# Kernel optimization log

Hardware: AMD Instinct MI355X
Metric: run time of the kernel (lower is better)

## Reference

```python
import jax, jax.numpy as jnp
import numpy as np

# Constants mirroring __init__ kwargs
SOURCE_LABEL = 2.0
SINK_LABEL = 3.0
GM_LABEL = 1.0  # hard-coded as `image == 1` in the torch module
THRESH = 0.05
MAX_ITERS = 500


def setup_inputs() -> dict:
    key = jax.random.key(0)
    # Label volume: 0=background, 1=gray matter, 2=source, 3=sink
    image = jax.random.randint(key, (2, 1, 64, 64, 64), 0, 4).astype(jnp.float32)
    return {"image": image}


def _solve(image):
    bs = image.shape[0]
    # squeeze channel, zero-pad each volume by 1 voxel, concat along axis 0
    vol = jnp.pad(image[:, 0], ((0, 0), (1, 1), (1, 1), (1, 1)))  # (bs, D+2, H+2, W+2)
    vol = vol.reshape(-1, vol.shape[2], vol.shape[3])              # (bs*(D+2), H+2, W+2)
    h, w, d = vol.shape
    wopt = 2.0 / (1.0 + np.pi / float(min(h, w, d)))

    # boundary conditions: 0 at source (already 0), 1 at sink
    init = jnp.where(vol == SINK_LABEL, 1.0, 0.0).astype(jnp.float32)

    # red-black coloring restricted to gray-matter voxels
    ii, jj, kk = jnp.meshgrid(jnp.arange(h), jnp.arange(w), jnp.arange(d), indexing="ij")
    parity = (ii + jj + kk) % 2
    gm = (vol == GM_LABEL)
    black = ((parity == 0) & gm).ravel()
    red = ((parity == 1) & gm).ravel()

    flat0 = init.ravel()

    def nbsum(x):
        # flat-index neighbor gathers x[i-1], x[i+1], x[i-d], x[i+d], x[i-d*w], x[i+d*w]
        # roll(x, s)[i] == x[i - s]; colored voxels never sit at flat boundaries
        return (jnp.roll(x, 1) + jnp.roll(x, -1)
                + jnp.roll(x, d) + jnp.roll(x, -d)
                + jnp.roll(x, d * w) + jnp.roll(x, -d * w))

    def half_step(x, mask):
        adj = wopt * (nbsum(x) - 6.0 * x) / 6.0
        x_new = jnp.where(mask, x + adj, x)
        dv = jnp.sum(jnp.abs(jnp.where(mask, adj, 0.0)))
        return x_new, dv

    def body(carry):
        x, it, _ = carry
        x, dv_b = half_step(x, black)   # black sweep uses pre-sweep values
        x, dv_r = half_step(x, red)     # red sweep uses updated black values
        return x, it + 1, dv_b + dv_r

    def cond(carry):
        _, it, dv = carry
        # torch loop breaks when delta_v < thresh or iterations > 500 (checked post-body)
        return (it == 0) | ((dv >= THRESH) & (it <= MAX_ITERS))

    x, iters, dv = jax.lax.while_loop(
        cond, body, (flat0, jnp.int32(0), jnp.float32(0.0)))

    # split concatenated solution back per-volume and crop the padding
    lap = x.reshape(bs, h // bs, w, d)[:, 1:-1, 1:-1, 1:-1][:, None]  # (bs,1,D,H,W)
    return lap, iters, dv


def reference(image):
    return _solve(image)
```

## Files before the change

### kernel.cpp

```cpp
#include <hip/hip_runtime.h>
#include <cstdint>


#define NBLK 132
#define NTHR 1024
#define NW   (NTHR / 64)

constexpr int NJK   = 66;
constexpr int PLANE = 66 * 66;
constexpr int HPL   = PLANE / 2;
constexpr int NI    = 132;
constexpr int CAPL  = 2048;
constexpr int NOUT  = 2 * 64 * 64 * 64;
constexpr int CTRL_U64 = 408 * 16;
constexpr unsigned long long CNT1   = 1ull << 44;
constexpr unsigned long long MASK44 = CNT1 - 1ull;

__global__ void sor_init_ctrl(unsigned long long* ctrl) {
  for (int i = threadIdx.x; i < CTRL_U64; i += blockDim.x) ctrl[i] = 0ull;
}

__device__ __forceinline__ float cloadf(const float* p) {
  return __hip_atomic_load(p, __ATOMIC_RELAXED, __HIP_MEMORY_SCOPE_AGENT);
}
__device__ __forceinline__ void cstoref(float* p, float v) {
  __hip_atomic_store(p, v, __ATOMIC_RELAXED, __HIP_MEMORY_SCOPE_AGENT);
}
__device__ __forceinline__ unsigned long long cloadu(const unsigned long long* p) {
  return __hip_atomic_load(p, __ATOMIC_RELAXED, __HIP_MEMORY_SCOPE_AGENT);
}
__device__ __forceinline__ void cstoreu(unsigned long long* p, unsigned long long v) {
  __hip_atomic_store(p, v, __ATOMIC_RELAXED, __HIP_MEMORY_SCOPE_AGENT);
}

__device__ __forceinline__ int pad_label_idx(int ii, int jj, int kk) {
  int b  = (ii >= 66) ? 1 : 0;
  int pz = ii - 66 * b;
  if (pz < 1 || pz > 64 || jj < 1 || jj > 64 || kk < 1 || kk > 64) return -1;
  return ((b * 64 + (pz - 1)) * 64 + (jj - 1)) * 64 + (kk - 1);
}

__global__ __launch_bounds__(NTHR, 1)
void sor_main(const float* __restrict__ img,
              float* __restrict__ pb0, float* __restrict__ pb1,
              float* __restrict__ pr0, float* __restrict__ pr1,
              unsigned long long* __restrict__ ctrl,
              float* __restrict__ out) {
  __shared__ double P1[PLANE];
  __shared__ unsigned lsB[CAPL], lsR[CAPL];
  __shared__ unsigned wsum[NW], woff[NW];
  __shared__ unsigned tot;
  __shared__ double redw[NW];
  __shared__ unsigned long long prevs[8];
  __shared__ double sh_dv;

  const int tid = threadIdx.x, bid = blockIdx.x;
  const int lane = tid & 63, wid = tid >> 6;
  const int z = bid;
  const int zm = (z > 0) ? (z - 1) : z;
  const int zp = (z < NI - 1) ? (z + 1) : z;

  for (int o = tid; o < PLANE; o += NTHR) {
    int j = o / NJK, k = o - j * NJK;
    int li = pad_label_idx(z, j, k);
    float L = (li >= 0) ? img[li] : 0.0f;
    P1[o] = (L == 3.0f) ? 1.0 : 0.0;
  }
  if (tid < 8) prevs[tid] = 0ull;

  int cntB = 0, cntR = 0;
  const int CH = (PLANE + NTHR - 1) / NTHR;
  for (int pass = 0; pass < 2; ++pass) {
    unsigned* list = (pass == 0) ? lsB : lsR;
    int c0 = tid * CH;
    int c1 = (c0 + CH < PLANE) ? (c0 + CH) : PLANE;
    unsigned cnt = 0;
    for (int o = c0; o < c1; ++o) {
      int j = o / NJK, k = o - j * NJK;
      if (((z + j + k) & 1) != pass) continue;
      int li = pad_label_idx(z, j, k);
      float L = (li >= 0) ? img[li] : 0.0f;
      if (L == 1.0f) cnt++;
    }
    unsigned incl = cnt;
    #pragma unroll
    for (int m = 1; m < 64; m <<= 1) {
      unsigned t = __shfl_up(incl, m, 64);
      if (lane >= m) incl += t;
    }
    __syncthreads();
    if (lane == 63) wsum[wid] = incl;
    __syncthreads();
    if (tid == 0) {
      unsigned a = 0;
      for (int w = 0; w < NW; ++w) { unsigned c = wsum[w]; woff[w] = a; a += c; }
      tot = a;
    }
    __syncthreads();
    unsigned p = (incl - cnt) + woff[wid];
    for (int o = c0; o < c1; ++o) {
      int j = o / NJK, k = o - j * NJK;
      if (((z + j + k) & 1) != pass) continue;
      int li = pad_label_idx(z, j, k);
      float L = (li >= 0) ? img[li] : 0.0f;
      if (L == 1.0f)
        list[p++] = (unsigned)o | ((unsigned)(33 * j + (k >> 1)) << 16);
    }
    __syncthreads();
    if (pass == 0) cntB = (int)tot; else cntR = (int)tot;
  }

  for (int c = tid; c < HPL; c += NTHR) {
    int j = c / 33, m = c - 33 * j;
    int kb = (m << 1) + ((z + j) & 1);
    int kr = (m << 1) + ((z + j + 1) & 1);
    float vb = (float)P1[NJK * j + kb];
    float vr = (float)P1[NJK * j + kr];
    cstoref(&pb0[(size_t)z * HPL + c], vb);
    cstoref(&pb1[(size_t)z * HPL + c], vb);
    cstoref(&pr0[(size_t)z * HPL + c], vr);
    cstoref(&pr1[(size_t)z * HPL + c], vr);
  }
  __syncthreads();
  if (tid == 0)
    __hip_atomic_fetch_add(&ctrl[(128u + (unsigned)(bid & 15)) * 16u], 1ull,
                           __ATOMIC_RELAXED, __HIP_MEMORY_SCOPE_AGENT);
  if (tid < 16) {
    for (;;) {
      unsigned long long v = cloadu(&ctrl[(128u + (unsigned)tid) * 16u]);
      v += __shfl_xor(v, 1, 64);  v += __shfl_xor(v, 2, 64);
      v += __shfl_xor(v, 4, 64);  v += __shfl_xor(v, 8, 64);
      if (v >= (unsigned long long)NBLK) break;
      __builtin_amdgcn_s_sleep(1);
    }
  }
  __syncthreads();

  const double WOPT = 2.0 / (1.0 + 3.14159265358979323846 / 66.0);

  int itout = 0;
  double dvout = 0.0;

  for (int t = 1; t <= 555; ++t) {
    const float* __restrict__ prold = (t & 1) ? pr0 : pr1;
    float* __restrict__ pbcur       = (t & 1) ? pb1 : pb0;
    float* __restrict__ prcur       = (t & 1) ? pr1 : pr0;

    if (t > 1) {
      const int g = t - 2;
      if (wid == 0 && lane < 2) {
        int nz = (lane == 0) ? (z - 1) : (z + 1);
        if (nz >= 0 && nz < NI) {
          while (cloadu(&ctrl[(276u + (unsigned)nz) * 16u])
                 < (unsigned long long)(t - 1))
            __builtin_amdgcn_s_sleep(1);
        }
      }
      if (g >= 1 && wid == 1 && lane < 16) {
        const int r = g & 7;
        const unsigned n = ((unsigned)g + 7u) >> 3;
        const unsigned long long t64 =
            ((unsigned long long)(132u * n)) << 44;
        unsigned long long v;
        for (;;) {
          v = cloadu(&ctrl[((unsigned)r * 16u + (unsigned)lane) * 16u]);
          v += __shfl_xor(v, 1, 64);  v += __shfl_xor(v, 2, 64);
          v += __shfl_xor(v, 4, 64);  v += __shfl_xor(v, 8, 64);
          if (v >= t64) break;
          __builtin_amdgcn_s_sleep(1);
        }
        if (lane == 0) {
          unsigned long long cum = v & MASK44;
          sh_dv = (double)(cum - prevs[r]) * (1.0 / 1048576.0);
          prevs[r] = cum;
        }
      }
      __syncthreads();
      if (g >= 1) {
        double dvg = sh_dv;
        if (!((dvg >= 0.05) && (g <= 500))) { itout = g; dvout = dvg; break; }
      }
    }

    double acc = 0.0;
    {
      const float* __restrict__ rm = prold + (size_t)zm * HPL;
      const float* __restrict__ rp = prold + (size_t)zp * HPL;
      float* __restrict__ pbz = pbcur + (size_t)z * HPL;
      for (int p = tid; p < cntB; p += NTHR) {
        const unsigned e = lsB[p];
        const int o = (int)(e & 0xFFFFu);
        const int c = (int)(e >> 16);
        float fzm = cloadf(&rm[c]);
        float fzp = cloadf(&rp[c]);
        double xi = P1[o];
        double nb = ((((P1[o - 1] + P1[o + 1]) + P1[o - NJK]) + P1[o + NJK])
                    + (double)fzm) + (double)fzp;
        double adj = (WOPT * (nb - 6.0 * xi)) / 6.0;
        double v = xi + adj;
        P1[o] = v;
        cstoref(&pbz[c], (float)v);
        acc += fabs(adj);
      }
    }
    __syncthreads();
    if (tid == 0)
      cstoreu(&ctrl[(144u + (unsigned)z) * 16u], (unsigned long long)t);
    if (tid < 2) {
      int nz = (tid == 0) ? (z - 1) : (z + 1);
      if (nz >= 0 && nz < NI) {
        while (cloadu(&ctrl[(144u + (unsigned)nz) * 16u])
               < (unsigned long long)t)
          __builtin_amdgcn_s_sleep(1);
      }
    }
    __syncthreads();

    {
      const float* __restrict__ bm = pbcur + (size_t)zm * HPL;
      const float* __restrict__ bp = pbcur + (size_t)zp * HPL;
      float* __restrict__ prz = prcur + (size_t)z * HPL;
      for (int p = tid; p < cntR; p += NTHR) {
        const unsigned e = lsR[p];
        const int o = (int)(e & 0xFFFFu);
        const int c = (int)(e >> 16);
        float fzm = cloadf(&bm[c]);
        float fzp = cloadf(&bp[c]);
        double xi = P1[o];
        double nb = ((((P1[o - 1] + P1[o + 1]) + P1[o - NJK]) + P1[o + NJK])
                    + (double)fzm) + (double)fzp;
        double adj = (WOPT * (nb - 6.0 * xi)) / 6.0;
        double v = xi + adj;
        P1[o] = v;
        cstoref(&prz[c], (float)v);
        acc += fabs(adj);
      }
    }

    double a = acc;
    #pragma unroll
    for (int m = 32; m >= 1; m >>= 1) a += __shfl_xor(a, m, 64);
    if (lane == 0) redw[wid] = a;
    __syncthreads();
    if (tid == 0) {
      double s = redw[0];
      #pragma unroll
      for (int w = 1; w < NW; ++w) s += redw[w];
      cstoreu(&ctrl[(276u + (unsigned)z) * 16u], (unsigned long long)t);
      __hip_atomic_fetch_add(
          &ctrl[(((unsigned)t & 7u) * 16u + (unsigned)(bid & 15)) * 16u],
          CNT1 + (unsigned long long)(s * 1048576.0 + 0.5),
          __ATOMIC_RELAXED, __HIP_MEMORY_SCOPE_AGENT);
    }
  }

  {
    const int vb = (z >= 66) ? 1 : 0;
    const int pz = z - 66 * vb;
    if (pz >= 1 && pz <= 64) {
      float* ob = out + ((size_t)vb * 64 + (pz - 1)) * 4096;
      for (int t2 = tid; t2 < 4096; t2 += NTHR) {
        int jj = t2 >> 6, kk = t2 & 63;
        ob[t2] = (float)P1[NJK * (jj + 1) + (kk + 1)];
      }
    }
    if (z == 0 && tid == 0) {
      out[NOUT]     = (float)itout;
      out[NOUT + 1] = (float)dvout;
    }
  }
}

extern "C" void kernel_launch(void* const* d_in, const int* in_sizes, int n_in,
                              void* d_out, int out_size, void* d_ws, size_t ws_size,
                              hipStream_t stream) {
  const float* img = (const float*)d_in[0];
  float* out = (float*)d_out;
  float* pb0 = (float*)d_ws;
  float* pb1 = pb0 + (size_t)NI * HPL;
  float* pr0 = pb1 + (size_t)NI * HPL;
  float* pr1 = pr0 + (size_t)NI * HPL;
  unsigned long long* ctrl = (unsigned long long*)(pr1 + (size_t)NI * HPL);

  sor_init_ctrl<<<1, 256, 0, stream>>>(ctrl);
  sor_main<<<NBLK, NTHR, 0, stream>>>(img, pb0, pb1, pr0, pr1, ctrl, out);
}
```

Before: 523.9 us.

## Assign three z-planes per block so interior plane stays in LDS

```diff
diff --git a/kernel.cpp b/kernel.cpp
--- a/kernel.cpp
+++ b/kernel.cpp
@@ -2,7 +2,7 @@
 #include <cstdint>
 
 
-#define NBLK 132
+#define NBLK 44
 #define NTHR 1024
 #define NW   (NTHR / 64)
 
@@ -46,80 +46,89 @@
               float* __restrict__ pr0, float* __restrict__ pr1,
               unsigned long long* __restrict__ ctrl,
               float* __restrict__ out) {
-  __shared__ double P1[PLANE];
-  __shared__ unsigned lsB[CAPL], lsR[CAPL];
+  __shared__ double P[3][PLANE];
+  __shared__ unsigned short ls[3][2][CAPL];
   __shared__ unsigned wsum[NW], woff[NW];
   __shared__ unsigned tot;
+  __shared__ unsigned cnts[3][2];
   __shared__ double redw[NW];
   __shared__ unsigned long long prevs[8];
   __shared__ double sh_dv;
 
   const int tid = threadIdx.x, bid = blockIdx.x;
   const int lane = tid & 63, wid = tid >> 6;
-  const int z = bid;
-  const int zm = (z > 0) ? (z - 1) : z;
-  const int zp = (z < NI - 1) ? (z + 1) : z;
-
-  for (int o = tid; o < PLANE; o += NTHR) {
-    int j = o / NJK, k = o - j * NJK;
-    int li = pad_label_idx(z, j, k);
-    float L = (li >= 0) ? img[li] : 0.0f;
-    P1[o] = (L == 3.0f) ? 1.0 : 0.0;
-  }
-  if (tid < 8) prevs[tid] = 0ull;
-
-  int cntB = 0, cntR = 0;
-  const int CH = (PLANE + NTHR - 1) / NTHR;
-  for (int pass = 0; pass < 2; ++pass) {
-    unsigned* list = (pass == 0) ? lsB : lsR;
-    int c0 = tid * CH;
-    int c1 = (c0 + CH < PLANE) ? (c0 + CH) : PLANE;
-    unsigned cnt = 0;
-    for (int o = c0; o < c1; ++o) {
+  const int z0 = 3 * bid;
+
+  for (int s = 0; s < 3; ++s) {
+    const int z = z0 + s;
+    for (int o = tid; o < PLANE; o += NTHR) {
       int j = o / NJK, k = o - j * NJK;
-      if (((z + j + k) & 1) != pass) continue;
       int li = pad_label_idx(z, j, k);
       float L = (li >= 0) ? img[li] : 0.0f;
-      if (L == 1.0f) cnt++;
-    }
-    unsigned incl = cnt;
-    #pragma unroll
-    for (int m = 1; m < 64; m <<= 1) {
-      unsigned t = __shfl_up(incl, m, 64);
-      if (lane >= m) incl += t;
-    }
-    __syncthreads();
-    if (lane == 63) wsum[wid] = incl;
-    __syncthreads();
-    if (tid == 0) {
-      unsigned a = 0;
-      for (int w = 0; w < NW; ++w) { unsigned c = wsum[w]; woff[w] = a; a += c; }
-      tot = a;
-    }
-    __syncthreads();
-    unsigned p = (incl - cnt) + woff[wid];
-    for (int o = c0; o < c1; ++o) {
-      int j = o / NJK, k = o - j * NJK;
-      if (((z + j + k) & 1) != pass) continue;
-      int li = pad_label_idx(z, j, k);
-      float L = (li >= 0) ? img[li] : 0.0f;
-      if (L == 1.0f)
-        list[p++] = (unsigned)o | ((unsigned)(33 * j + (k >> 1)) << 16);
-    }
-    __syncthreads();
-    if (pass == 0) cntB = (int)tot; else cntR = (int)tot;
-  }
-
-  for (int c = tid; c < HPL; c += NTHR) {
-    int j = c / 33, m = c - 33 * j;
-    int kb = (m << 1) + ((z + j) & 1);
-    int kr = (m << 1) + ((z + j + 1) & 1);
-    float vb = (float)P1[NJK * j + kb];
-    float vr = (float)P1[NJK * j + kr];
-    cstoref(&pb0[(size_t)z * HPL + c], vb);
-    cstoref(&pb1[(size_t)z * HPL + c], vb);
-    cstoref(&pr0[(size_t)z * HPL + c], vr);
-    cstoref(&pr1[(size_t)z * HPL + c], vr);
+      P[s][o] = (L == 3.0f) ? 1.0 : 0.0;
+    }
+  }
+  if (tid < 8) prevs[tid] = 0ull;
+
+  const int CH = (PLANE + NTHR - 1) / NTHR;
+  for (int s = 0; s < 3; ++s) {
+    const int z = z0 + s;
+    for (int cb = 0; cb < 2; ++cb) {
+      unsigned short* list = ls[s][cb];
+      int c0 = tid * CH;
+      int c1 = (c0 + CH < PLANE) ? (c0 + CH) : PLANE;
+      unsigned cnt = 0;
+      for (int o = c0; o < c1; ++o) {
+        int j = o / NJK, k = o - j * NJK;
+        if (((z + j + k) & 1) != cb) continue;
+        int li = pad_label_idx(z, j, k);
+        float L = (li >= 0) ? img[li] : 0.0f;
+        if (L == 1.0f) cnt++;
+      }
+      unsigned incl = cnt;
+      #pragma unroll
+      for (int m = 1; m < 64; m <<= 1) {
+        unsigned t = __shfl_up(incl, m, 64);
+        if (lane >= m) incl += t;
+      }
+      __syncthreads();
+      if (lane == 63) wsum[wid] = incl;
+      __syncthreads();
+      if (tid == 0) {
+        unsigned a = 0;
+        for (int w = 0; w < NW; ++w) { unsigned c = wsum[w]; woff[w] = a; a += c; }
+        tot = a;
+      }
+      __syncthreads();
+      unsigned p = (incl - cnt) + woff[wid];
+      for (int o = c0; o < c1; ++o) {
+        int j = o / NJK, k = o - j * NJK;
+        if (((z + j + k) & 1) != cb) continue;
+        int li = pad_label_idx(z, j, k);
+        float L = (li >= 0) ? img[li] : 0.0f;
+        if (L == 1.0f) list[p++] = (unsigned short)o;
+      }
+      __syncthreads();
+      if (tid == 0) cnts[s][cb] = tot;
+      __syncthreads();
+    }
+  }
+  const int cB0 = (int)cnts[0][0], cB1 = (int)cnts[1][0], cB2 = (int)cnts[2][0];
+  const int cR0 = (int)cnts[0][1], cR1 = (int)cnts[1][1], cR2 = (int)cnts[2][1];
+
+  for (int s = 0; s < 3; s += 2) {
+    const int z = z0 + s;
+    for (int c = tid; c < HPL; c += NTHR) {
+      int j = c / 33, m = c - 33 * j;
+      int kb = (m << 1) + ((z + j) & 1);
+      int kr = (m << 1) + ((z + j + 1) & 1);
+      float vb = (float)P[s][NJK * j + kb];
+      float vr = (float)P[s][NJK * j + kr];
+      cstoref(&pb0[(size_t)z * HPL + c], vb);
+      cstoref(&pb1[(size_t)z * HPL + c], vb);
+      cstoref(&pr0[(size_t)z * HPL + c], vr);
+      cstoref(&pr1[(size_t)z * HPL + c], vr);
+    }
   }
   __syncthreads();
   if (tid == 0)
@@ -149,9 +158,9 @@
     if (t > 1) {
       const int g = t - 2;
       if (wid == 0 && lane < 2) {
-        int nz = (lane == 0) ? (z - 1) : (z + 1);
-        if (nz >= 0 && nz < NI) {
-          while (cloadu(&ctrl[(276u + (unsigned)nz) * 16u])
+        int nb = (lane == 0) ? (bid - 1) : (bid + 1);
+        if (nb >= 0 && nb < NBLK) {
+          while (cloadu(&ctrl[(276u + (unsigned)nb) * 16u])
                  < (unsigned long long)(t - 1))
             __builtin_amdgcn_s_sleep(1);
         }
@@ -160,7 +169,7 @@
         const int r = g & 7;
         const unsigned n = ((unsigned)g + 7u) >> 3;
         const unsigned long long t64 =
-            ((unsigned long long)(132u * n)) << 44;
+            ((unsigned long long)NBLK * n) << 44;
         unsigned long long v;
         for (;;) {
           v = cloadu(&ctrl[((unsigned)r * 16u + (unsigned)lane) * 16u]);
@@ -184,32 +193,83 @@
 
     double acc = 0.0;
     {
-      const float* __restrict__ rm = prold + (size_t)zm * HPL;
-      const float* __restrict__ rp = prold + (size_t)zp * HPL;
-      float* __restrict__ pbz = pbcur + (size_t)z * HPL;
-      for (int p = tid; p < cntB; p += NTHR) {
-        const unsigned e = lsB[p];
-        const int o = (int)(e & 0xFFFFu);
-        const int c = (int)(e >> 16);
-        float fzm = cloadf(&rm[c]);
-        float fzp = cloadf(&rp[c]);
-        double xi = P1[o];
-        double nb = ((((P1[o - 1] + P1[o + 1]) + P1[o - NJK]) + P1[o + NJK])
-                    + (double)fzm) + (double)fzp;
-        double adj = (WOPT * (nb - 6.0 * xi)) / 6.0;
-        double v = xi + adj;
-        P1[o] = v;
-        cstoref(&pbz[c], (float)v);
+      const float* __restrict__ rmz =
+          (z0 > 0) ? (prold + (size_t)(z0 - 1) * HPL) : prold;
+      const float* __restrict__ rpz =
+          (z0 + 3 < NI) ? (prold + (size_t)(z0 + 3) * HPL) : prold;
+      float g0a = 0, g0b = 0, g2a = 0, g2b = 0;
+      int o0a = -1, o0b = -1, o2a = -1, o2b = -1;
+      if (tid < cB0)        { o0a = (int)ls[0][0][tid];
+                              g0a = cloadf(&rmz[o0a >> 1]); }
+      if (tid + 1024 < cB0) { o0b = (int)ls[0][0][tid + 1024];
+                              g0b = cloadf(&rmz[o0b >> 1]); }
+      if (tid < cB2)        { o2a = (int)ls[2][0][tid];
+                              g2a = cloadf(&rpz[o2a >> 1]); }
+      if (tid + 1024 < cB2) { o2b = (int)ls[2][0][tid + 1024];
+                              g2b = cloadf(&rpz[o2b >> 1]); }
+      for (int p = tid; p < cB1; p += NTHR) {
+        const int o = (int)ls[1][0][p];
+        double xi = P[1][o];
+        double nb = ((((P[1][o - 1] + P[1][o + 1]) + P[1][o - NJK])
+                    + P[1][o + NJK]) + P[0][o]) + P[2][o];
+        double adj = (WOPT * (nb - 6.0 * xi)) / 6.0;
+        P[1][o] = xi + adj;
+        acc += fabs(adj);
+      }
+      float* __restrict__ pbz0 = pbcur + (size_t)z0 * HPL;
+      if (o0a >= 0) {
+        const int o = o0a;
+        double xi = P[0][o];
+        double nb = ((((P[0][o - 1] + P[0][o + 1]) + P[0][o - NJK])
+                    + P[0][o + NJK]) + (double)g0a) + P[1][o];
+        double adj = (WOPT * (nb - 6.0 * xi)) / 6.0;
+        double v = xi + adj;
+        P[0][o] = v;
+        cstoref(&pbz0[o >> 1], (float)v);
+        acc += fabs(adj);
+      }
+      if (o0b >= 0) {
+        const int o = o0b;
+        double xi = P[0][o];
+        double nb = ((((P[0][o - 1] + P[0][o + 1]) + P[0][o - NJK])
+                    + P[0][o + NJK]) + (double)g0b) + P[1][o];
+        double adj = (WOPT * (nb - 6.0 * xi)) / 6.0;
+        double v = xi + adj;
+        P[0][o] = v;
+        cstoref(&pbz0[o >> 1], (float)v);
+        acc += fabs(adj);
+      }
+      float* __restrict__ pbz2 = pbcur + (size_t)(z0 + 2) * HPL;
+      if (o2a >= 0) {
+        const int o = o2a;
+        double xi = P[2][o];
+        double nb = ((((P[2][o - 1] + P[2][o + 1]) + P[2][o - NJK])
+                    + P[2][o + NJK]) + P[1][o]) + (double)g2a;
+        double adj = (WOPT * (nb - 6.0 * xi)) / 6.0;
+        double v = xi + adj;
+        P[2][o] = v;
+        cstoref(&pbz2[o >> 1], (float)v);
+        acc += fabs(adj);
+      }
+      if (o2b >= 0) {
+        const int o = o2b;
+        double xi = P[2][o];
+        double nb = ((((P[2][o - 1] + P[2][o + 1]) + P[2][o - NJK])
+                    + P[2][o + NJK]) + P[1][o]) + (double)g2b;
+        double adj = (WOPT * (nb - 6.0 * xi)) / 6.0;
+        double v = xi + adj;
+        P[2][o] = v;
+        cstoref(&pbz2[o >> 1], (float)v);
         acc += fabs(adj);
       }
     }
     __syncthreads();
     if (tid == 0)
-      cstoreu(&ctrl[(144u + (unsigned)z) * 16u], (unsigned long long)t);
+      cstoreu(&ctrl[(144u + (unsigned)bid) * 16u], (unsigned long long)t);
     if (tid < 2) {
-      int nz = (tid == 0) ? (z - 1) : (z + 1);
-      if (nz >= 0 && nz < NI) {
-        while (cloadu(&ctrl[(144u + (unsigned)nz) * 16u])
+      int nb = (tid == 0) ? (bid - 1) : (bid + 1);
+      if (nb >= 0 && nb < NBLK) {
+        while (cloadu(&ctrl[(144u + (unsigned)nb) * 16u])
                < (unsigned long long)t)
           __builtin_amdgcn_s_sleep(1);
       }
@@ -217,22 +277,73 @@
     __syncthreads();
 
     {
-      const float* __restrict__ bm = pbcur + (size_t)zm * HPL;
-      const float* __restrict__ bp = pbcur + (size_t)zp * HPL;
-      float* __restrict__ prz = prcur + (size_t)z * HPL;
-      for (int p = tid; p < cntR; p += NTHR) {
-        const unsigned e = lsR[p];
-        const int o = (int)(e & 0xFFFFu);
-        const int c = (int)(e >> 16);
-        float fzm = cloadf(&bm[c]);
-        float fzp = cloadf(&bp[c]);
-        double xi = P1[o];
-        double nb = ((((P1[o - 1] + P1[o + 1]) + P1[o - NJK]) + P1[o + NJK])
-                    + (double)fzm) + (double)fzp;
-        double adj = (WOPT * (nb - 6.0 * xi)) / 6.0;
-        double v = xi + adj;
-        P1[o] = v;
-        cstoref(&prz[c], (float)v);
+      const float* __restrict__ bmz =
+          (z0 > 0) ? (pbcur + (size_t)(z0 - 1) * HPL) : pbcur;
+      const float* __restrict__ bpz =
+          (z0 + 3 < NI) ? (pbcur + (size_t)(z0 + 3) * HPL) : pbcur;
+      float g0a = 0, g0b = 0, g2a = 0, g2b = 0;
+      int o0a = -1, o0b = -1, o2a = -1, o2b = -1;
+      if (tid < cR0)        { o0a = (int)ls[0][1][tid];
+                              g0a = cloadf(&bmz[o0a >> 1]); }
+      if (tid + 1024 < cR0) { o0b = (int)ls[0][1][tid + 1024];
+                              g0b = cloadf(&bmz[o0b >> 1]); }
+      if (tid < cR2)        { o2a = (int)ls[2][1][tid];
+                              g2a = cloadf(&bpz[o2a >> 1]); }
+      if (tid + 1024 < cR2) { o2b = (int)ls[2][1][tid + 1024];
+                              g2b = cloadf(&bpz[o2b >> 1]); }
+      for (int p = tid; p < cR1; p += NTHR) {
+        const int o = (int)ls[1][1][p];
+        double xi = P[1][o];
+        double nb = ((((P[1][o - 1] + P[1][o + 1]) + P[1][o - NJK])
+                    + P[1][o + NJK]) + P[0][o]) + P[2][o];
+        double adj = (WOPT * (nb - 6.0 * xi)) / 6.0;
+        P[1][o] = xi + adj;
+        acc += fabs(adj);
+      }
+      float* __restrict__ prz0 = prcur + (size_t)z0 * HPL;
+      if (o0a >= 0) {
+        const int o = o0a;
+        double xi = P[0][o];
+        double nb = ((((P[0][o - 1] + P[0][o + 1]) + P[0][o - NJK])
+                    + P[0][o + NJK]) + (double)g0a) + P[1][o];
+        double adj = (WOPT * (nb - 6.0 * xi)) / 6.0;
+        double v = xi + adj;
+        P[0][o] = v;
+        cstoref(&prz0[o >> 1], (float)v);
+        acc += fabs(adj);
+      }
+      if (o0b >= 0) {
+        const int o = o0b;
+        double xi = P[0][o];
+        double nb = ((((P[0][o - 1] + P[0][o + 1]) + P[0][o - NJK])
+                    + P[0][o + NJK]) + (double)g0b) + P[1][o];
+        double adj = (WOPT * (nb - 6.0 * xi)) / 6.0;
+        double v = xi + adj;
+        P[0][o] = v;
+        cstoref(&prz0[o >> 1], (float)v);
+        acc += fabs(adj);
+      }
+      float* __restrict__ prz2 = prcur + (size_t)(z0 + 2) * HPL;
+      if (o2a >= 0) {
+        const int o = o2a;
+        double xi = P[2][o];
+        double nb = ((((P[2][o - 1] + P[2][o + 1]) + P[2][o - NJK])
+                    + P[2][o + NJK]) + P[1][o]) + (double)g2a;
+        double adj = (WOPT * (nb - 6.0 * xi)) / 6.0;
+        double v = xi + adj;
+        P[2][o] = v;
+        cstoref(&prz2[o >> 1], (float)v);
+        acc += fabs(adj);
+      }
+      if (o2b >= 0) {
+        const int o = o2b;
+        double xi = P[2][o];
+        double nb = ((((P[2][o - 1] + P[2][o + 1]) + P[2][o - NJK])
+                    + P[2][o + NJK]) + P[1][o]) + (double)g2b;
+        double adj = (WOPT * (nb - 6.0 * xi)) / 6.0;
+        double v = xi + adj;
+        P[2][o] = v;
+        cstoref(&prz2[o >> 1], (float)v);
         acc += fabs(adj);
       }
     }
@@ -246,7 +357,7 @@
       double s = redw[0];
       #pragma unroll
       for (int w = 1; w < NW; ++w) s += redw[w];
-      cstoreu(&ctrl[(276u + (unsigned)z) * 16u], (unsigned long long)t);
+      cstoreu(&ctrl[(276u + (unsigned)bid) * 16u], (unsigned long long)t);
       __hip_atomic_fetch_add(
           &ctrl[(((unsigned)t & 7u) * 16u + (unsigned)(bid & 15)) * 16u],
           CNT1 + (unsigned long long)(s * 1048576.0 + 0.5),
@@ -254,20 +365,21 @@
     }
   }
 
-  {
+  for (int s = 0; s < 3; ++s) {
+    const int z = z0 + s;
     const int vb = (z >= 66) ? 1 : 0;
     const int pz = z - 66 * vb;
     if (pz >= 1 && pz <= 64) {
       float* ob = out + ((size_t)vb * 64 + (pz - 1)) * 4096;
       for (int t2 = tid; t2 < 4096; t2 += NTHR) {
         int jj = t2 >> 6, kk = t2 & 63;
-        ob[t2] = (float)P1[NJK * (jj + 1) + (kk + 1)];
-      }
-    }
-    if (z == 0 && tid == 0) {
-      out[NOUT]     = (float)itout;
-      out[NOUT + 1] = (float)dvout;
-    }
+        ob[t2] = (float)P[s][NJK * (jj + 1) + (kk + 1)];
+      }
+    }
+  }
+  if (bid == 0 && tid == 0) {
+    out[NOUT]     = (float)itout;
+    out[NOUT + 1] = (float)dvout;
   }
 }
 
```

New measurement: 803.1 us. 1.53x slower.
